# Kernel tuning notes

Measured on AMD Instinct MI355X. Metric: run time of the kernel, lower is better.

## Reference

```python
import jax, jax.numpy as jnp
import numpy as np

B, V, J, NS, NE = 2048, 5023, 5, 100, 50
PB = 9 * (J - 1)  # pose basis = 36


def setup_inputs() -> dict:
    key = jax.random.key(0)
    ks = jax.random.split(key, 8)
    jr = jax.random.uniform(ks[5], (J, V), dtype=jnp.float32)
    lw = jax.random.uniform(ks[6], (V, J), dtype=jnp.float32)
    return {
        "shape_params": jax.random.normal(ks[0], (B, NS), dtype=jnp.float32),
        "expression_params": jax.random.normal(ks[1], (B, NE), dtype=jnp.float32),
        "pose": jax.random.normal(ks[2], (B, J * 3), dtype=jnp.float32) * 0.2,
        "v_template": jax.random.normal(ks[3], (V, 3), dtype=jnp.float32) * 0.1,
        "shapedirs": jax.random.normal(ks[4], (V, 3, NS + NE), dtype=jnp.float32) * 0.01,
        "posedirs": jax.random.normal(ks[7], (PB, V * 3), dtype=jnp.float32) * 0.01,
        "J_regressor": jr / jnp.sum(jr, axis=1, keepdims=True),   # rows sum to 1 (convex combos)
        "lbs_weights": lw / jnp.sum(lw, axis=1, keepdims=True),   # rows sum to 1 (skinning weights)
        "parents": np.array([0, 0, 1, 1, 1], dtype=np.int64),     # FLAME kintree (root entry unused)
    }


def batch_rodrigues(rot_vecs):
    """(N,3) axis-angle -> (N,3,3) rotation matrices (matches torch ref incl. +1e-8)."""
    angle = jnp.linalg.norm(rot_vecs + 1e-8, axis=1, keepdims=True)      # (N,1)
    rd = rot_vecs / angle
    cos = jnp.cos(angle)[:, :, None]                                      # (N,1,1)
    sin = jnp.sin(angle)[:, :, None]
    rx, ry, rz = rd[:, 0], rd[:, 1], rd[:, 2]
    z = jnp.zeros_like(rx)
    K = jnp.stack([z, -rz, ry, rz, z, -rx, -ry, rx, z], axis=1).reshape(-1, 3, 3)
    I = jnp.eye(3, dtype=rot_vecs.dtype)
    return I + sin * K + (1.0 - cos) * jnp.matmul(K, K)


def reference(shape_params, expression_params, pose, v_template, shapedirs,
              posedirs, J_regressor, lbs_weights, parents):
    par = np.asarray(parents)  # static kinematic tree
    b = shape_params.shape[0]
    betas = jnp.concatenate([shape_params, expression_params], axis=1)     # (B,150)
    v_shaped = v_template + jnp.einsum('bl,vkl->bvk', betas, shapedirs)    # (B,V,3)
    Jts = jnp.einsum('bvk,jv->bjk', v_shaped, J_regressor)                 # (B,J,3)
    # pose -> rotations, pose-corrective offsets
    rot_mats = batch_rodrigues(pose.reshape(-1, 3)).reshape(b, -1, 3, 3)   # (B,J,3,3)
    I3 = jnp.eye(3, dtype=pose.dtype)
    pose_feature = (rot_mats[:, 1:] - I3).reshape(b, -1)                   # (B,36)
    pose_offsets = jnp.matmul(pose_feature, posedirs).reshape(b, -1, 3)    # (B,V,3)
    v_posed = v_posed = pose_offsets + v_shaped
    # kinematic chain (relative joint transforms -> world transforms)
    rel_joints = jnp.concatenate(
        [Jts[:, :1], Jts[:, 1:] - Jts[:, par[1:]]], axis=1)                # (B,J,3)
    top = jnp.concatenate([rot_mats, rel_joints[..., None]], axis=-1)      # (B,J,3,4)
    bottom = jnp.broadcast_to(
        jnp.array([0., 0., 0., 1.], dtype=pose.dtype), (b, Jts.shape[1], 1, 4))
    tm = jnp.concatenate([top, bottom], axis=2)                            # (B,J,4,4)
    chain = [tm[:, 0]]
    for i in range(1, par.shape[0]):  # tiny fixed loop over 5 joints
        chain.append(jnp.matmul(chain[int(par[i])], tm[:, i]))
    transforms = jnp.stack(chain, axis=1)                                  # (B,J,4,4)
    posed_joints = transforms[:, :, :3, 3]
    # remove rest-pose joint locations: subtract (transforms @ [j;0]) from last column
    tj = jnp.einsum('bjmn,bjn->bjm', transforms[:, :, :, :3], Jts)         # (B,J,4)
    rel_transforms = transforms.at[:, :, :, 3].add(-tj)                    # (B,J,4,4)
    # linear blend skinning
    T = jnp.einsum('vj,bjmn->bvmn', lbs_weights, rel_transforms)           # (B,V,4,4)
    verts = jnp.einsum('bvmn,bvn->bvm', T[:, :, :3, :3], v_posed) + T[:, :, :3, 3]
    return verts, posed_joints
```

## Files before the change

### kernel.cpp

```cpp
#include <hip/hip_runtime.h>
#include <hip/hip_bf16.h>
#include <math.h>

#define B_N 2048
#define V_N 5023
#define V3_N 15069
#define NSJB 157
#define CHUNK 32

typedef float f32x4 __attribute__((ext_vector_type(4)));
typedef short short8 __attribute__((ext_vector_type(8)));

static __device__ __forceinline__ ushort f2bf(float f) {
  __hip_bfloat16 h = __float2bfloat16(f);
  return *reinterpret_cast<ushort*>(&h);
}

__global__ __launch_bounds__(256) void k_pre(const float* __restrict__ sdirs,
                                             const float* __restrict__ pdirs,
                                             const float* __restrict__ vtemp,
                                             const float* __restrict__ Jr,
                                             const float* __restrict__ shp,
                                             const float* __restrict__ expr,
                                             ushort* __restrict__ basis,
                                             float* __restrict__ SJ,
                                             ushort* __restrict__ bb) {
  __shared__ float Sh[16][452];
  __shared__ float Pd[36][48];
  int t = threadIdx.x, blk = blockIdx.x;
  if (blk < 314) {
    int bx = blk, v0 = bx * 16;
    for (int idx = t; idx < 16 * 450; idx += 256) {
      int r = idx / 450, c = idx - r * 450;
      int v = v0 + r;
      Sh[r][c] = (v < V_N) ? sdirs[(size_t)v * 450 + c] : 0.0f;
    }
    for (int idx = t; idx < 36 * 48; idx += 256) {
      int p = idx / 48, c = idx - p * 48;
      int v3 = v0 * 3 + c;
      Pd[p][c] = (v3 < V3_N) ? pdirs[(size_t)p * V3_N + v3] : 0.0f;
    }
    __syncthreads();
    for (int idx = t; idx < 64 * 96; idx += 256) {
      int row = idx / 96, kp = idx - row * 96;
      int vl = row >> 2, c = row & 3;
      int k0 = kp * 2;
      float f0 = 0.0f, f1 = 0.0f;
      if (c < 3) {
        if (k0 < 150) {
          f0 = Sh[vl][c * 150 + k0];
          f1 = Sh[vl][c * 150 + k0 + 1];
        } else if (k0 < 186) {
          f0 = Pd[k0 - 150][vl * 3 + c];
          f1 = Pd[k0 - 149][vl * 3 + c];
        }
      }
      uint u = (uint)f2bf(f0) | ((uint)f2bf(f1) << 16);
      ((uint*)basis)[(size_t)(bx * 64 + row) * 96 + kp] = u;
    }
  } else if (blk < 314 + NSJB) {
    float (*JrL)[CHUNK] = (float(*)[CHUNK]) & Sh[0][0];
    int bk = blk - 314;
    int vstart = bk * CHUNK;
    int cnt = min(CHUNK, V_N - vstart);
    for (int idx = t; idx < 5 * CHUNK; idx += 256) {
      int j = idx / CHUNK, vi = idx % CHUNK;
      JrL[j][vi] = (vi < cnt) ? Jr[j * V_N + vstart + vi] : 0.0f;
    }
    __syncthreads();
    float acc0[5] = {0, 0, 0, 0, 0}, acc1[5] = {0, 0, 0, 0, 0};
    int c0 = t, c1 = t + 256;
#pragma unroll 4
    for (int vi = 0; vi < CHUNK; ++vi) {
      int v = min(vstart + vi, V_N - 1);
      float val0 = sdirs[(size_t)v * 450 + c0];
      float val1 = 0.0f;
      if (c1 < 450) val1 = sdirs[(size_t)v * 450 + c1];
      else if (c1 < 453) val1 = vtemp[(size_t)v * 3 + (c1 - 450)];
#pragma unroll
      for (int j = 0; j < 5; ++j) {
        float w = JrL[j][vi];
        acc0[j] = fmaf(w, val0, acc0[j]);
        acc1[j] = fmaf(w, val1, acc1[j]);
      }
    }
#pragma unroll
    for (int j = 0; j < 5; ++j) {
      atomicAdd(&SJ[j * 456 + c0], acc0[j]);
      if (c1 < 453) atomicAdd(&SJ[j * 456 + c1], acc1[j]);
    }
  } else {
    int idx = (blk - 314 - NSJB) * 256 + t;
    int b = idx / 96, cp = idx - b * 96;
    int c0 = cp * 2;
    float f0 = 0.0f, f1 = 0.0f;
    if (c0 < 100) {
      f0 = shp[(size_t)b * 100 + c0];
      f1 = shp[(size_t)b * 100 + c0 + 1];
    } else if (c0 < 150) {
      f0 = expr[(size_t)b * 50 + (c0 - 100)];
      f1 = expr[(size_t)b * 50 + (c0 - 99)];
    }
    ((uint*)bb)[idx] = (uint)f2bf(f0) | ((uint)f2bf(f1) << 16);
  }
}

__global__ __launch_bounds__(256) void k_jpose(const float* __restrict__ shp,
                                               const float* __restrict__ expr,
                                               const float* __restrict__ SJ,
                                               const float* __restrict__ pose,
                                               ushort* __restrict__ bb,
                                               float* __restrict__ A,
                                               float* __restrict__ out) {
  __shared__ float JtL[16][16];
  int t = threadIdx.x;
  int g = t >> 4, r = t & 15;
  int b = blockIdx.x * 16 + g;
  if (r < 15) {
    int j = r / 3, k = r - j * 3;
    const float* SJr = SJ + j * 456;
    float acc = SJr[450 + k];
    const float* srow = shp + (size_t)b * 100;
    const float* erow = expr + (size_t)b * 50;
    for (int l = 0; l < 100; ++l) acc = fmaf(srow[l], SJr[k * 150 + l], acc);
    for (int l = 0; l < 50; ++l) acc = fmaf(erow[l], SJr[k * 150 + 100 + l], acc);
    JtL[g][r] = acc;
  }
  __syncthreads();
  if (r != 0) return;
  float R[5][3][3];
#pragma unroll
  for (int j = 0; j < 5; ++j) {
    float rx = pose[(size_t)b * 15 + j * 3 + 0];
    float ry = pose[(size_t)b * 15 + j * 3 + 1];
    float rz = pose[(size_t)b * 15 + j * 3 + 2];
    float sx = rx + 1e-8f, sy = ry + 1e-8f, sz = rz + 1e-8f;
    float ang = sqrtf(sx * sx + sy * sy + sz * sz);
    float inv = 1.0f / ang;
    float ux = rx * inv, uy = ry * inv, uz = rz * inv;
    float c = cosf(ang), s = sinf(ang), omc = 1.0f - c;
    float K[3][3] = {{0.0f, -uz, uy}, {uz, 0.0f, -ux}, {-uy, ux, 0.0f}};
#pragma unroll
    for (int m = 0; m < 3; ++m)
#pragma unroll
      for (int n = 0; n < 3; ++n) {
        float k2 = 0.0f;
#pragma unroll
        for (int q = 0; q < 3; ++q) k2 += K[m][q] * K[q][n];
        R[j][m][n] = ((m == n) ? 1.0f : 0.0f) + s * K[m][n] + omc * k2;
      }
  }
  {
    float pf[36];
#pragma unroll
    for (int j = 1; j < 5; ++j)
#pragma unroll
      for (int m = 0; m < 3; ++m)
#pragma unroll
        for (int n = 0; n < 3; ++n)
          pf[(j - 1) * 9 + m * 3 + n] = R[j][m][n] - ((m == n) ? 1.0f : 0.0f);
    uint* bbu = (uint*)bb + (size_t)b * 96 + 75;
#pragma unroll
    for (int q = 0; q < 18; ++q)
      bbu[q] = (uint)f2bf(pf[2 * q]) | ((uint)f2bf(pf[2 * q + 1]) << 16);
  }
  float Jt[5][3];
#pragma unroll
  for (int j = 0; j < 5; ++j)
#pragma unroll
    for (int k = 0; k < 3; ++k) Jt[j][k] = JtL[g][j * 3 + k];
  const int par[5] = {0, 0, 1, 1, 1};
  float rel[5][3];
#pragma unroll
  for (int k = 0; k < 3; ++k) rel[0][k] = Jt[0][k];
#pragma unroll
  for (int j = 1; j < 5; ++j)
#pragma unroll
    for (int k = 0; k < 3; ++k) rel[j][k] = Jt[j][k] - Jt[par[j]][k];
  float Rg[5][3][3], tg[5][3];
#pragma unroll
  for (int m = 0; m < 3; ++m) {
#pragma unroll
    for (int n = 0; n < 3; ++n) Rg[0][m][n] = R[0][m][n];
    tg[0][m] = rel[0][m];
  }
#pragma unroll
  for (int j = 1; j < 5; ++j) {
    int p = par[j];
#pragma unroll
    for (int m = 0; m < 3; ++m) {
      float t2 = tg[p][m];
#pragma unroll
      for (int n = 0; n < 3; ++n) {
        float s = 0.0f;
#pragma unroll
        for (int q = 0; q < 3; ++q) s = fmaf(Rg[p][m][q], R[j][q][n], s);
        Rg[j][m][n] = s;
        t2 = fmaf(Rg[p][m][n], rel[j][n], t2);
      }
      tg[j][m] = t2;
    }
  }
#pragma unroll
  for (int j = 0; j < 5; ++j)
#pragma unroll
    for (int k = 0; k < 3; ++k)
      out[(size_t)B_N * V_N * 3 + ((size_t)b * 5 + j) * 3 + k] = tg[j][k];
  float Af[5][12];
#pragma unroll
  for (int j = 0; j < 5; ++j)
#pragma unroll
    for (int m = 0; m < 3; ++m) {
      float tj = 0.0f;
#pragma unroll
      for (int n = 0; n < 3; ++n) {
        Af[j][m * 4 + n] = Rg[j][m][n];
        tj = fmaf(Rg[j][m][n], Jt[j][n], tj);
      }
      Af[j][m * 4 + 3] = tg[j][m] - tj;
    }
  float* Ab = A + (size_t)b * 64;
#pragma unroll
  for (int q = 0; q < 12; ++q) Ab[q] = Af[0][q];
#pragma unroll
  for (int j = 1; j < 5; ++j)
#pragma unroll
    for (int q = 0; q < 12; ++q) Ab[j * 12 + q] = Af[j][q] - Af[0][q];
}

__global__ __launch_bounds__(512, 6) void k_main(const ushort* __restrict__ basis,
                                                 const ushort* __restrict__ bb,
                                                 const float* __restrict__ Amat,
                                                 const float* __restrict__ lw,
                                                 const float* __restrict__ vtemp,
                                                 float* __restrict__ out) {
  __shared__ alignas(16) ushort AL[64 * 192];
  __shared__ alignas(16) ushort BL[64 * 192];
  float* AmL = (float*)AL;
  int t = threadIdx.x;
  int bx = blockIdx.y;
  int by = blockIdx.x;
  int b0 = by * 64;
#pragma unroll
  for (int i = 0; i < 3; ++i) {
    int c = t + i * 512;
    int r = c / 24, kb = c % 24;
    int dst = (r * 24 + (kb ^ (r & 7))) * 8;
    *(short8*)(&AL[dst]) = *(const short8*)(&basis[((size_t)bx * 64 + r) * 192 + kb * 8]);
    *(short8*)(&BL[dst]) = *(const short8*)(&bb[((size_t)(b0 + r)) * 192 + kb * 8]);
  }
  __syncthreads();
  int lane = t & 63;
  int w = __builtin_amdgcn_readfirstlane(t >> 6);
  int wm = w >> 1, wn = w & 1;
  int lm = lane & 15, g = lane >> 4;
  f32x4 acc0 = {0.f, 0.f, 0.f, 0.f}, acc1 = {0.f, 0.f, 0.f, 0.f};
  const int ar = wm * 16 + lm;
  const int br0 = wn * 32 + lm;
  const int br1 = wn * 32 + 16 + lm;
#pragma unroll
  for (int ks = 0; ks < 6; ++ks) {
    int kb = ks * 4 + g;
    short8 af = *(const short8*)(&AL[(ar * 24 + (kb ^ (ar & 7))) * 8]);
    short8 bf0 = *(const short8*)(&BL[(br0 * 24 + (kb ^ (br0 & 7))) * 8]);
    short8 bf1 = *(const short8*)(&BL[(br1 * 24 + (kb ^ (br1 & 7))) * 8]);
    acc0 = __builtin_amdgcn_mfma_f32_16x16x32_bf16(af, bf0, acc0, 0, 0, 0);
    acc1 = __builtin_amdgcn_mfma_f32_16x16x32_bf16(af, bf1, acc1, 0, 0, 0);
  }
  int v = bx * 16 + wm * 4 + g;
  bool valid = v < V_N;
  int vv = valid ? v : 0;
  float wv[4];
#pragma unroll
  for (int j = 0; j < 4; ++j) wv[j] = lw[(size_t)vv * 5 + 1 + j];
  float vt0 = vtemp[(size_t)vv * 3 + 0];
  float vt1 = vtemp[(size_t)vv * 3 + 1];
  float vt2 = vtemp[(size_t)vv * 3 + 2];
  __syncthreads();
#pragma unroll
  for (int i = 0; i < 2; ++i) {
    int c = t + i * 512;
    int r = c / 16, q = (c % 16) * 4;
    *(f32x4*)(&AmL[r * 68 + q]) = *(const f32x4*)(&Amat[((size_t)(b0 + r)) * 64 + q]);
  }
  __syncthreads();
#pragma unroll
  for (int ni = 0; ni < 2; ++ni) {
    f32x4 p = ni ? acc1 : acc0;
    int bl = wn * 32 + ni * 16 + lm;
    const float* Ar = &AmL[bl * 68];
    f32x4 T0 = *(const f32x4*)(Ar + 0);
    f32x4 T1 = *(const f32x4*)(Ar + 4);
    f32x4 T2 = *(const f32x4*)(Ar + 8);
#pragma unroll
    for (int j = 1; j < 5; ++j) {
      f32x4 d0 = *(const f32x4*)(Ar + j * 12 + 0);
      f32x4 d1 = *(const f32x4*)(Ar + j * 12 + 4);
      f32x4 d2 = *(const f32x4*)(Ar + j * 12 + 8);
      float wjv = wv[j - 1];
#pragma unroll
      for (int c = 0; c < 4; ++c) {
        T0[c] = fmaf(wjv, d0[c], T0[c]);
        T1[c] = fmaf(wjv, d1[c], T1[c]);
        T2[c] = fmaf(wjv, d2[c], T2[c]);
      }
    }
    float x = p[0] + vt0, y = p[1] + vt1, z = p[2] + vt2;
    float ox = fmaf(T0[0], x, fmaf(T0[1], y, fmaf(T0[2], z, T0[3])));
    float oy = fmaf(T1[0], x, fmaf(T1[1], y, fmaf(T1[2], z, T1[3])));
    float oz = fmaf(T2[0], x, fmaf(T2[1], y, fmaf(T2[2], z, T2[3])));
    if (valid) {
      size_t o = ((size_t)(b0 + bl)) * V3_N + (size_t)v * 3;
      out[o + 0] = ox;
      out[o + 1] = oy;
      out[o + 2] = oz;
    }
  }
}

extern "C" void kernel_launch(void* const* d_in, const int* in_sizes, int n_in,
                              void* d_out, int out_size, void* d_ws, size_t ws_size,
                              hipStream_t stream) {
  const float* shp = (const float*)d_in[0];
  const float* expr = (const float*)d_in[1];
  const float* pose = (const float*)d_in[2];
  const float* vtemp = (const float*)d_in[3];
  const float* sdirs = (const float*)d_in[4];
  const float* pdirs = (const float*)d_in[5];
  const float* Jr = (const float*)d_in[6];
  const float* lw = (const float*)d_in[7];
  float* out = (float*)d_out;
  float* wsf = (float*)d_ws;

  const size_t OFF_SJ = 358400;
  const size_t OFF_A = 786688;
  const size_t OFF_BB = 917760;
  const size_t OFF_BASIS = 1114368;
  float* SJ = wsf + OFF_SJ;
  float* A = wsf + OFF_A;
  ushort* bb = (ushort*)(wsf + OFF_BB);
  ushort* basis = (ushort*)(wsf + OFF_BASIS);

  hipMemsetAsync(SJ, 0, 2280 * sizeof(float), stream);
  hipLaunchKernelGGL(k_pre, dim3(314 + NSJB + 768), dim3(256), 0, stream,
                     sdirs, pdirs, vtemp, Jr, shp, expr, basis, SJ, bb);
  hipLaunchKernelGGL(k_jpose, dim3(128), dim3(256), 0, stream,
                     shp, expr, SJ, pose, bb, A, out);
  hipLaunchKernelGGL(k_main, dim3(32, 314), dim3(512), 0, stream,
                     basis, bb, A, lw, vtemp, out);
}
```

Measured before the change: 111.7 us.

## Pre-swizzle operand layouts and load LDS tiles via direct global-to-LDS copies

The producer kernels now write the basis and batch-coefficient matrices in the XOR-swizzled order the main GEMM kernel expects. This lets k_main copy tiles straight into LDS with global_load_lds instead of going through registers and computing swizzled addresses on the fly. The hipMemsetAsync for the joint accumulator is replaced by a tiny zeroing kernel. The layout now has to stay consistent across three kernels, and the zeroing kernel adds one more launch.

```diff
diff --git a/kernel.cpp b/kernel.cpp
--- a/kernel.cpp
+++ b/kernel.cpp
@@ -14,6 +14,11 @@
 static __device__ __forceinline__ ushort f2bf(float f) {
   __hip_bfloat16 h = __float2bfloat16(f);
   return *reinterpret_cast<ushort*>(&h);
+}
+
+__global__ void k_zero(float* __restrict__ SJ) {
+  int id = blockIdx.x * 256 + threadIdx.x;
+  if (id < 2280) SJ[id] = 0.0f;
 }
 
 __global__ __launch_bounds__(256) void k_pre(const float* __restrict__ sdirs,
@@ -56,7 +61,8 @@
         }
       }
       uint u = (uint)f2bf(f0) | ((uint)f2bf(f1) << 16);
-      ((uint*)basis)[(size_t)(bx * 64 + row) * 96 + kp] = u;
+      int kb = kp >> 2, e = kp & 3;
+      ((uint*)basis)[(size_t)(bx * 64 + row) * 96 + (((kb ^ (row & 7)) << 2) + e)] = u;
     }
   } else if (blk < 314 + NSJB) {
     float (*JrL)[CHUNK] = (float(*)[CHUNK]) & Sh[0][0];
@@ -101,7 +107,10 @@
       f0 = expr[(size_t)b * 50 + (c0 - 100)];
       f1 = expr[(size_t)b * 50 + (c0 - 99)];
     }
-    ((uint*)bb)[idx] = (uint)f2bf(f0) | ((uint)f2bf(f1) << 16);
+    int r = b & 63;
+    int kb = cp >> 2, e = cp & 3;
+    ((uint*)bb)[(size_t)b * 96 + (((kb ^ (r & 7)) << 2) + e)] =
+        (uint)f2bf(f0) | ((uint)f2bf(f1) << 16);
   }
 }
 
@@ -159,10 +168,14 @@
 #pragma unroll
         for (int n = 0; n < 3; ++n)
           pf[(j - 1) * 9 + m * 3 + n] = R[j][m][n] - ((m == n) ? 1.0f : 0.0f);
-    uint* bbu = (uint*)bb + (size_t)b * 96 + 75;
-#pragma unroll
-    for (int q = 0; q < 18; ++q)
-      bbu[q] = (uint)f2bf(pf[2 * q]) | ((uint)f2bf(pf[2 * q + 1]) << 16);
+    uint* bbu = (uint*)bb + (size_t)b * 96;
+    int rr = b & 7;
+#pragma unroll
+    for (int q = 0; q < 18; ++q) {
+      int cp = 75 + q;
+      int kb = cp >> 2, e = cp & 3;
+      bbu[((kb ^ rr) << 2) + e] = (uint)f2bf(pf[2 * q]) | ((uint)f2bf(pf[2 * q + 1]) << 16);
+    }
   }
   float Jt[5][3];
 #pragma unroll
@@ -241,17 +254,24 @@
   int bx = blockIdx.y;
   int by = blockIdx.x;
   int b0 = by * 64;
-#pragma unroll
-  for (int i = 0; i < 3; ++i) {
-    int c = t + i * 512;
-    int r = c / 24, kb = c % 24;
-    int dst = (r * 24 + (kb ^ (r & 7))) * 8;
-    *(short8*)(&AL[dst]) = *(const short8*)(&basis[((size_t)bx * 64 + r) * 192 + kb * 8]);
-    *(short8*)(&BL[dst]) = *(const short8*)(&bb[((size_t)(b0 + r)) * 192 + kb * 8]);
-  }
-  __syncthreads();
   int lane = t & 63;
   int w = __builtin_amdgcn_readfirstlane(t >> 6);
+  {
+    const char* gA = (const char*)(basis + (size_t)bx * 64 * 192);
+    const char* gB = (const char*)(bb + (size_t)b0 * 192);
+#pragma unroll
+    for (int i = 0; i < 3; ++i) {
+      int chunk = w * 3 + i;
+      int off = chunk * 1024 + lane * 16;
+      __builtin_amdgcn_global_load_lds(
+          (const __attribute__((address_space(1))) uint*)(gA + off),
+          (__attribute__((address_space(3))) uint*)((char*)&AL[0] + chunk * 1024), 16, 0, 0);
+      __builtin_amdgcn_global_load_lds(
+          (const __attribute__((address_space(1))) uint*)(gB + off),
+          (__attribute__((address_space(3))) uint*)((char*)&BL[0] + chunk * 1024), 16, 0, 0);
+    }
+  }
+  __syncthreads();
   int wm = w >> 1, wn = w & 1;
   int lm = lane & 15, g = lane >> 4;
   f32x4 acc0 = {0.f, 0.f, 0.f, 0.f}, acc1 = {0.f, 0.f, 0.f, 0.f};
@@ -341,7 +361,7 @@
   ushort* bb = (ushort*)(wsf + OFF_BB);
   ushort* basis = (ushort*)(wsf + OFF_BASIS);
 
-  hipMemsetAsync(SJ, 0, 2280 * sizeof(float), stream);
+  hipLaunchKernelGGL(k_zero, dim3(9), dim3(256), 0, stream, SJ);
   hipLaunchKernelGGL(k_pre, dim3(314 + NSJB + 768), dim3(256), 0, stream,
                      sdirs, pdirs, vtemp, Jr, shp, expr, basis, SJ, bb);
   hipLaunchKernelGGL(k_jpose, dim3(128), dim3(256), 0, stream,
```

Result: faster. 108.3 us (median of 2 runs) (-3.0%).
